# Optimization experiments

Hardware: AMD Instinct MI355X
Metric: run time of the kernel (lower is better)

The kernel has to match this reference:

```python
import jax, jax.numpy as jnp
import numpy as np

N_NODES = 20000
N_EDGES = 320000
T = 8
C_IN = 32
C_OUT = 32
C_EDGE = 16


def setup_inputs() -> dict:
    key = jax.random.key(0)
    ks = jax.random.split(key, 10)

    def xavier(k, shape):
        fan_in, fan_out = shape[0], shape[1]
        limit = float(np.sqrt(6.0 / (fan_in + fan_out)))
        return jax.random.uniform(k, shape, jnp.float32, -limit, limit)

    X = jax.random.normal(ks[0], (N_NODES, T, C_IN), jnp.float32)
    edge_index = jax.random.randint(ks[1], (2, N_EDGES), 0, N_NODES, jnp.int32)
    edge_attr = jax.random.normal(ks[2], (N_EDGES, C_EDGE), jnp.float32)
    Wn1 = xavier(ks[3], (C_IN, C_OUT))
    We1 = xavier(ks[4], (C_EDGE, C_OUT))
    u1 = xavier(ks[5], (C_OUT, C_OUT))
    Wn2 = xavier(ks[6], (C_OUT, C_OUT))
    We2 = xavier(ks[7], (C_EDGE, C_OUT))
    u2 = xavier(ks[8], (C_OUT, C_OUT))
    return {"X": X, "edge_index": edge_index, "edge_attr": edge_attr,
            "Wn1": Wn1, "We1": We1, "u1": u1,
            "Wn2": Wn2, "We2": We2, "u2": u2}


def _gat_conv(x, edge_index, edge_attr, Wn, We, u):
    # x: [N, T, C_in] -> h: [N, T, C_out]
    h = jnp.matmul(x, Wn)
    _ea = jnp.matmul(edge_attr, We)  # computed in original forward, unused in message (dead code)
    # per-edge matmul with u == node-level matmul then gather (same math, cheaper)
    hu = jnp.matmul(h, u)  # [N, T, C]
    src, tgt = edge_index[0], edge_index[1]
    x_j = hu[src]  # [E, T, C]
    x_i = hu[tgt]  # [E, T, C]
    gate = jax.nn.sigmoid(jnp.sum(x_i * x_j, axis=-1, keepdims=True))  # [E, T, 1]
    msg = x_j * gate  # [E, T, C]
    agg = jax.ops.segment_max(msg, tgt, num_segments=N_NODES)  # max-aggregate into targets
    agg = jnp.where(jnp.isfinite(agg), agg, jnp.zeros((), agg.dtype))  # empty segments -> 0 (PyG fill)
    return h + agg  # residual update


def reference(X, edge_index, edge_attr, Wn1, We1, u1, Wn2, We2, u2):
    c1 = jax.nn.leaky_relu(_gat_conv(X, edge_index, edge_attr, Wn1, We1, u1), 0.01)
    c2 = jax.nn.leaky_relu(_gat_conv(c1, edge_index, edge_attr, Wn2, We2, u2), 0.01)
    return c2
```

## Files before the change

### kernel.cpp

```cpp
#include <hip/hip_runtime.h>
#include <hip/hip_fp16.h>
#include <cstdint>
#include <cstddef>
#include <math.h>

#define NNODES 20000
#define NEDGES 320000
#define TDIM   8
#define CDIM   32
#define RROWS  (NNODES * TDIM)
#define NELEM  (RROWS * CDIM)
#define NODEB  79

static __device__ __forceinline__ unsigned pk2(float a, float b) {
    __half2 h = __floats2half2_rn(a, b);
    return *reinterpret_cast<unsigned*>(&h);
}

static __device__ __forceinline__ void cvt8(uint4 r, float* a) {
    float2 f;
    f = __half22float2(*reinterpret_cast<__half2*>(&r.x)); a[0] = f.x; a[1] = f.y;
    f = __half22float2(*reinterpret_cast<__half2*>(&r.y)); a[2] = f.x; a[3] = f.y;
    f = __half22float2(*reinterpret_cast<__half2*>(&r.z)); a[4] = f.x; a[5] = f.y;
    f = __half22float2(*reinterpret_cast<__half2*>(&r.w)); a[6] = f.x; a[7] = f.y;
}

__global__ __launch_bounds__(256) void init_kernel(
    const float* __restrict__ Wn1, const float* __restrict__ u1, float* __restrict__ WU1,
    const float* __restrict__ Wn2, const float* __restrict__ u2, float* __restrict__ WU2,
    int* __restrict__ counts)
{
    int blk = blockIdx.x, tid = threadIdx.x;
    if (blk < NODEB) {
        int i = blk * 256 + tid;
        if (i < NNODES) counts[i] = 0;
        return;
    }
    int b = blk - NODEB;
    const float* W  = (b < 4) ? Wn1 : Wn2;
    const float* U  = (b < 4) ? u1  : u2;
    float*       WU = (b < 4) ? WU1 : WU2;
    int idx = (b & 3) * 256 + tid;
    int k = idx >> 5, c = idx & 31;
    float acc = 0.f;
#pragma unroll
    for (int j = 0; j < CDIM; ++j) acc = fmaf(W[k * CDIM + j], U[j * CDIM + c], acc);
    WU[idx] = acc;
}

__global__ __launch_bounds__(256) void hist_kernel(
    const int* __restrict__ ei, int* __restrict__ counts)
{
    int e = blockIdx.x * 256 + threadIdx.x;
    if (e < NEDGES) atomicAdd(&counts[ei[NEDGES + e]], 1);
}

__global__ __launch_bounds__(256) void scan_kernel(
    const int* __restrict__ counts,
    int* __restrict__ offsets, int* __restrict__ cursor)
{
    __shared__ int sd[256];
    int blk = blockIdx.x, tid = threadIdx.x;

    int pre = 0;
    for (int i = tid; i < blk * 256; i += 256) pre += counts[i];
    sd[tid] = pre;
    __syncthreads();
#pragma unroll
    for (int off = 128; off > 0; off >>= 1) {
        if (tid < off) sd[tid] += sd[tid + off];
        __syncthreads();
    }
    int base = sd[0];
    __syncthreads();

    int i = blk * 256 + tid;
    int v = (i < NNODES) ? counts[i] : 0;
    sd[tid] = v;
    __syncthreads();
#pragma unroll
    for (int off = 1; off < 256; off <<= 1) {
        int t = (tid >= off) ? sd[tid - off] : 0;
        __syncthreads();
        sd[tid] += t;
        __syncthreads();
    }
    int excl = base + sd[tid] - v;
    if (i < NNODES) { offsets[i] = excl; cursor[i] = excl; }
    if (i == NNODES - 1) offsets[NNODES] = NEDGES;
}

__global__ __launch_bounds__(256) void scatter_kernel(
    const int* __restrict__ ei,
    int* __restrict__ cursor,
    int* __restrict__ csr_src)
{
    int e = blockIdx.x * 256 + threadIdx.x;
    if (e < NEDGES) {
        int t = ei[NEDGES + e];
        int pos = atomicAdd(&cursor[t], 1);
        csr_src[pos] = ei[e];
    }
}

template<bool IN16>
__global__ __launch_bounds__(256) void linear2_kernel(
    const void* __restrict__ inp,
    const float* __restrict__ W,
    const float* __restrict__ WU,
    __half* __restrict__ h16,
    __half* __restrict__ hu16)
{
    __shared__ float sx[64][33];
    int tid = threadIdx.x;
    int rowBase = blockIdx.x * 64;

    if (IN16) {
        const char* base = (const char*)inp + (size_t)rowBase * 64;
        uint4 v = *(const uint4*)(base + (size_t)tid * 16);
        float a[8];
        cvt8(v, a);
        int r = tid >> 2, q = tid & 3;
#pragma unroll
        for (int j = 0; j < 8; ++j) sx[r][q * 8 + j] = a[j];
    } else {
        const float4* in4 = (const float4*)((const float*)inp + (size_t)rowBase * CDIM);
#pragma unroll
        for (int i = 0; i < 2; ++i) {
            int idx = tid + i * 256;
            float4 v = in4[idx];
            int r = idx >> 3, q = idx & 7;
            sx[r][4 * q + 0] = v.x; sx[r][4 * q + 1] = v.y;
            sx[r][4 * q + 2] = v.z; sx[r][4 * q + 3] = v.w;
        }
    }
    __syncthreads();

    int lane  = tid & 63;
    int chunk = __builtin_amdgcn_readfirstlane(tid >> 6);
    int row = rowBase + lane;

    float hr[8], acc[8];
#pragma unroll
    for (int j = 0; j < 8; ++j) { hr[j] = 0.f; acc[j] = 0.f; }

    const float* Wc  = W  + chunk * 8;
    const float* WUc = WU + chunk * 8;
#pragma unroll 4
    for (int k = 0; k < CDIM; ++k) {
        float xk = sx[lane][k];
#pragma unroll
        for (int j = 0; j < 8; ++j) {
            hr[j]  = fmaf(xk, Wc[k * CDIM + j],  hr[j]);
            acc[j] = fmaf(xk, WUc[k * CDIM + j], acc[j]);
        }
    }

    uint4* hp = (uint4*)((char*)h16 + (size_t)row * 64 + chunk * 16);
    *hp = make_uint4(pk2(hr[0], hr[1]), pk2(hr[2], hr[3]),
                     pk2(hr[4], hr[5]), pk2(hr[6], hr[7]));

    uint4* up = (uint4*)((char*)hu16 + (size_t)row * 64 + chunk * 16);
    *up = make_uint4(pk2(acc[0], acc[1]), pk2(acc[2], acc[3]),
                     pk2(acc[4], acc[5]), pk2(acc[6], acc[7]));
}

template<bool OUT16>
__global__ __launch_bounds__(256) void agg_kernel(
    const int* __restrict__ offsets,
    const int* __restrict__ csr_src,
    const __half* __restrict__ hu16,
    const __half* __restrict__ h16,
    void* __restrict__ outp)
{
    int tid = threadIdx.x;
    int n = blockIdx.x * 4 + (tid >> 6);
    int l64 = tid & 63;
    int half = l64 >> 5;
    int l32 = l64 & 31;
    uint32_t rowOff = (uint32_t)l32 * 16u;
    const char* hub = (const char*)hu16;

    float b[8];
    cvt8(*(const uint4*)(hub + ((uint32_t)n << 9) + rowOff), b);

    int k0 = offsets[n];
    int k1 = offsets[n + 1];

    float m[8];
#pragma unroll
    for (int j = 0; j < 8; ++j) m[j] = -INFINITY;

    int k = k0;
    int e0 = 0, e1 = 0;
    if (k + 4 <= k1) {
        e0 = csr_src[k + half];
        e1 = csr_src[k + 2 + half];
    }
    while (k + 4 <= k1) {
        uint4 r0 = *(const uint4*)(hub + (((uint32_t)e0 << 9) + rowOff));
        uint4 r1 = *(const uint4*)(hub + (((uint32_t)e1 << 9) + rowOff));
        k += 4;
        if (k + 4 <= k1) {
            e0 = csr_src[k + half];
            e1 = csr_src[k + 2 + half];
        }
        float a0[8], a1[8];
        cvt8(r0, a0); cvt8(r1, a1);
        float q0 = 0.f, q1 = 0.f;
#pragma unroll
        for (int j = 0; j < 8; ++j) { q0 = fmaf(a0[j], b[j], q0); q1 = fmaf(a1[j], b[j], q1); }
        q0 += __shfl_xor(q0, 1); q1 += __shfl_xor(q1, 1);
        q0 += __shfl_xor(q0, 2); q1 += __shfl_xor(q1, 2);
        float g0 = 1.f / (1.f + __expf(-q0));
        float g1 = 1.f / (1.f + __expf(-q1));
#pragma unroll
        for (int j = 0; j < 8; ++j) {
            m[j] = fmaxf(m[j], a0[j] * g0);
            m[j] = fmaxf(m[j], a1[j] * g1);
        }
    }
    for (; k < k1; ++k) {
        int s = csr_src[k];
        float a0[8];
        cvt8(*(const uint4*)(hub + (((uint32_t)s << 9) + rowOff)), a0);
        float q0 = 0.f;
#pragma unroll
        for (int j = 0; j < 8; ++j) q0 = fmaf(a0[j], b[j], q0);
        q0 += __shfl_xor(q0, 1);
        q0 += __shfl_xor(q0, 2);
        float g0 = 1.f / (1.f + __expf(-q0));
#pragma unroll
        for (int j = 0; j < 8; ++j) m[j] = fmaxf(m[j], a0[j] * g0);
    }

#pragma unroll
    for (int j = 0; j < 8; ++j) m[j] = fmaxf(m[j], __shfl_xor(m[j], 32));

    if (half == 0) {
        bool has = (k1 > k0);
        float hv[8];
        cvt8(*(const uint4*)((const char*)h16 + ((uint32_t)n << 9) + rowOff), hv);
        float o[8];
#pragma unroll
        for (int j = 0; j < 8; ++j) {
            float a = has ? m[j] : 0.f;
            float vv = hv[j] + a;
            o[j] = (vv >= 0.f) ? vv : 0.01f * vv;
        }
        if (OUT16) {
            uint4 w = make_uint4(pk2(o[0], o[1]), pk2(o[2], o[3]),
                                 pk2(o[4], o[5]), pk2(o[6], o[7]));
            *(uint4*)((char*)outp + ((uint32_t)n << 9) + rowOff) = w;
        } else {
            uint32_t nodeOff = (uint32_t)n * 1024u + (uint32_t)l32 * 32u;
            char* ob = (char*)outp;
            *(float4*)(ob + nodeOff)      = make_float4(o[0], o[1], o[2], o[3]);
            *(float4*)(ob + nodeOff + 16) = make_float4(o[4], o[5], o[6], o[7]);
        }
    }
}

extern "C" void kernel_launch(void* const* d_in, const int* in_sizes, int n_in,
                              void* d_out, int out_size, void* d_ws, size_t ws_size,
                              hipStream_t stream)
{
    const float* X   = (const float*)d_in[0];
    const int*   ei  = (const int*)  d_in[1];
    const float* Wn1 = (const float*)d_in[3];
    const float* u1  = (const float*)d_in[5];
    const float* Wn2 = (const float*)d_in[6];
    const float* u2  = (const float*)d_in[8];

    int* counts  = (int*)d_ws;
    int* offsets = counts + NNODES;
    int* cursor  = offsets + NNODES + 1;
    float* WU1   = (float*)(cursor + NNODES);
    float* WU2   = WU1 + 1024;
    int* csr     = (int*)(WU2 + 1024);
    __half* A16  = (__half*)(((uintptr_t)(csr + NEDGES) + 255) & ~(uintptr_t)255);
    __half* Hh   = A16 + NELEM;
    __half* HU   = Hh + NELEM;

    const int linBlocks  = RROWS / 64;
    const int edgeBlocks = (NEDGES + 255) / 256;
    const int aggBlocks  = NNODES / 4;

    init_kernel<<<NODEB + 8, 256, 0, stream>>>(Wn1, u1, WU1, Wn2, u2, WU2, counts);
    hist_kernel<<<edgeBlocks, 256, 0, stream>>>(ei, counts);
    scan_kernel<<<NODEB, 256, 0, stream>>>(counts, offsets, cursor);
    scatter_kernel<<<edgeBlocks, 256, 0, stream>>>(ei, cursor, csr);

    linear2_kernel<false><<<linBlocks, 256, 0, stream>>>(X, Wn1, WU1, Hh, HU);
    agg_kernel<true><<<aggBlocks, 256, 0, stream>>>(offsets, csr, HU, Hh, A16);

    linear2_kernel<true><<<linBlocks, 256, 0, stream>>>(A16, Wn2, WU2, Hh, HU);
    agg_kernel<false><<<aggBlocks, 256, 0, stream>>>(offsets, csr, HU, Hh, d_out);
}
```

Measured before the change: 145.0 us.

## Fuse layer-1 aggregation with layer-2 linear transform in one kernel

Replaces the layer-1 aggregation kernel and the layer-2 linear kernel with a single fused kernel. Each 512-thread block aggregates 8 nodes, writes the leaky-relu output into shared memory, then computes the layer-2 h and hu projections directly from it. This drops the fp16 intermediate round trip through global memory and one kernel launch. Because the compute now follows a block-wide barrier, slow high-degree nodes can stall the whole block, and the larger 512-thread blocks may reduce occupancy.

```diff
diff --git a/kernel.cpp b/kernel.cpp
--- a/kernel.cpp
+++ b/kernel.cpp
@@ -103,9 +103,8 @@
     }
 }
 
-template<bool IN16>
 __global__ __launch_bounds__(256) void linear2_kernel(
-    const void* __restrict__ inp,
+    const float* __restrict__ in,
     const float* __restrict__ W,
     const float* __restrict__ WU,
     __half* __restrict__ h16,
@@ -115,24 +114,14 @@
     int tid = threadIdx.x;
     int rowBase = blockIdx.x * 64;
 
-    if (IN16) {
-        const char* base = (const char*)inp + (size_t)rowBase * 64;
-        uint4 v = *(const uint4*)(base + (size_t)tid * 16);
-        float a[8];
-        cvt8(v, a);
-        int r = tid >> 2, q = tid & 3;
-#pragma unroll
-        for (int j = 0; j < 8; ++j) sx[r][q * 8 + j] = a[j];
-    } else {
-        const float4* in4 = (const float4*)((const float*)inp + (size_t)rowBase * CDIM);
-#pragma unroll
-        for (int i = 0; i < 2; ++i) {
-            int idx = tid + i * 256;
-            float4 v = in4[idx];
-            int r = idx >> 3, q = idx & 7;
-            sx[r][4 * q + 0] = v.x; sx[r][4 * q + 1] = v.y;
-            sx[r][4 * q + 2] = v.z; sx[r][4 * q + 3] = v.w;
-        }
+    const float4* in4 = (const float4*)(in + (size_t)rowBase * CDIM);
+#pragma unroll
+    for (int i = 0; i < 2; ++i) {
+        int idx = tid + i * 256;
+        float4 v = in4[idx];
+        int r = idx >> 3, q = idx & 7;
+        sx[r][4 * q + 0] = v.x; sx[r][4 * q + 1] = v.y;
+        sx[r][4 * q + 2] = v.z; sx[r][4 * q + 3] = v.w;
     }
     __syncthreads();
 
@@ -159,19 +148,131 @@
     uint4* hp = (uint4*)((char*)h16 + (size_t)row * 64 + chunk * 16);
     *hp = make_uint4(pk2(hr[0], hr[1]), pk2(hr[2], hr[3]),
                      pk2(hr[4], hr[5]), pk2(hr[6], hr[7]));
-
     uint4* up = (uint4*)((char*)hu16 + (size_t)row * 64 + chunk * 16);
     *up = make_uint4(pk2(acc[0], acc[1]), pk2(acc[2], acc[3]),
                      pk2(acc[4], acc[5]), pk2(acc[6], acc[7]));
 }
 
-template<bool OUT16>
+__global__ __launch_bounds__(512) void aggfuse_kernel(
+    const int* __restrict__ offsets,
+    const int* __restrict__ csr_src,
+    const __half* __restrict__ hu16,
+    const __half* __restrict__ h16,
+    const float* __restrict__ W2,
+    const float* __restrict__ WU2,
+    __half* __restrict__ h2_16,
+    __half* __restrict__ hu2_16)
+{
+    __shared__ float sc1[64][33];
+    int tid = threadIdx.x;
+    int wid = tid >> 6;
+    int n = blockIdx.x * 8 + wid;
+    int l64 = tid & 63;
+    int half = l64 >> 5;
+    int l32 = l64 & 31;
+    uint32_t rowOff = (uint32_t)l32 * 16u;
+    const char* hub = (const char*)hu16;
+
+    float b[8];
+    cvt8(*(const uint4*)(hub + ((uint32_t)n << 9) + rowOff), b);
+
+    int k0 = offsets[n];
+    int k1 = offsets[n + 1];
+
+    float m[8];
+#pragma unroll
+    for (int j = 0; j < 8; ++j) m[j] = -INFINITY;
+
+    int k = k0;
+    int e0 = 0, e1 = 0;
+    if (k + 4 <= k1) {
+        e0 = csr_src[k + half];
+        e1 = csr_src[k + 2 + half];
+    }
+    while (k + 4 <= k1) {
+        uint4 r0 = *(const uint4*)(hub + (((uint32_t)e0 << 9) + rowOff));
+        uint4 r1 = *(const uint4*)(hub + (((uint32_t)e1 << 9) + rowOff));
+        k += 4;
+        if (k + 4 <= k1) {
+            e0 = csr_src[k + half];
+            e1 = csr_src[k + 2 + half];
+        }
+        float a0[8], a1[8];
+        cvt8(r0, a0); cvt8(r1, a1);
+        float q0 = 0.f, q1 = 0.f;
+#pragma unroll
+        for (int j = 0; j < 8; ++j) { q0 = fmaf(a0[j], b[j], q0); q1 = fmaf(a1[j], b[j], q1); }
+        q0 += __shfl_xor(q0, 1); q1 += __shfl_xor(q1, 1);
+        q0 += __shfl_xor(q0, 2); q1 += __shfl_xor(q1, 2);
+        float g0 = 1.f / (1.f + __expf(-q0));
+        float g1 = 1.f / (1.f + __expf(-q1));
+#pragma unroll
+        for (int j = 0; j < 8; ++j) {
+            m[j] = fmaxf(m[j], a0[j] * g0);
+            m[j] = fmaxf(m[j], a1[j] * g1);
+        }
+    }
+    for (; k < k1; ++k) {
+        int s = csr_src[k];
+        float a0[8];
+        cvt8(*(const uint4*)(hub + (((uint32_t)s << 9) + rowOff)), a0);
+        float q0 = 0.f;
+#pragma unroll
+        for (int j = 0; j < 8; ++j) q0 = fmaf(a0[j], b[j], q0);
+        q0 += __shfl_xor(q0, 1);
+        q0 += __shfl_xor(q0, 2);
+        float g0 = 1.f / (1.f + __expf(-q0));
+#pragma unroll
+        for (int j = 0; j < 8; ++j) m[j] = fmaxf(m[j], a0[j] * g0);
+    }
+
+#pragma unroll
+    for (int j = 0; j < 8; ++j) m[j] = fmaxf(m[j], __shfl_xor(m[j], 32));
+
+    if (half == 0) {
+        bool has = (k1 > k0);
+        float hv[8];
+        cvt8(*(const uint4*)((const char*)h16 + ((uint32_t)n << 9) + rowOff), hv);
+        int rloc = wid * 8 + (l32 >> 2);
+        int cbase = (l32 & 3) * 8;
+#pragma unroll
+        for (int j = 0; j < 8; ++j) {
+            float a = has ? m[j] : 0.f;
+            float vv = hv[j] + a;
+            sc1[rloc][cbase + j] = (vv >= 0.f) ? vv : 0.01f * vv;
+        }
+    }
+    __syncthreads();
+
+    int w = __builtin_amdgcn_readfirstlane(wid);
+    int r = l64;
+    float h2[4], a2[4];
+#pragma unroll
+    for (int j = 0; j < 4; ++j) { h2[j] = 0.f; a2[j] = 0.f; }
+
+    const float* Wc = W2  + w * 4;
+    const float* Uc = WU2 + w * 4;
+#pragma unroll 4
+    for (int kk = 0; kk < CDIM; ++kk) {
+        float xk = sc1[r][kk];
+#pragma unroll
+        for (int j = 0; j < 4; ++j) {
+            h2[j] = fmaf(xk, Wc[kk * CDIM + j], h2[j]);
+            a2[j] = fmaf(xk, Uc[kk * CDIM + j], a2[j]);
+        }
+    }
+
+    size_t rowg = (size_t)blockIdx.x * 64 + r;
+    *(uint2*)((char*)h2_16  + rowg * 64 + w * 8) = make_uint2(pk2(h2[0], h2[1]), pk2(h2[2], h2[3]));
+    *(uint2*)((char*)hu2_16 + rowg * 64 + w * 8) = make_uint2(pk2(a2[0], a2[1]), pk2(a2[2], a2[3]));
+}
+
 __global__ __launch_bounds__(256) void agg_kernel(
     const int* __restrict__ offsets,
     const int* __restrict__ csr_src,
     const __half* __restrict__ hu16,
     const __half* __restrict__ h16,
-    void* __restrict__ outp)
+    float* __restrict__ outp)
 {
     int tid = threadIdx.x;
     int n = blockIdx.x * 4 + (tid >> 6);
@@ -248,16 +349,10 @@
             float vv = hv[j] + a;
             o[j] = (vv >= 0.f) ? vv : 0.01f * vv;
         }
-        if (OUT16) {
-            uint4 w = make_uint4(pk2(o[0], o[1]), pk2(o[2], o[3]),
-                                 pk2(o[4], o[5]), pk2(o[6], o[7]));
-            *(uint4*)((char*)outp + ((uint32_t)n << 9) + rowOff) = w;
-        } else {
-            uint32_t nodeOff = (uint32_t)n * 1024u + (uint32_t)l32 * 32u;
-            char* ob = (char*)outp;
-            *(float4*)(ob + nodeOff)      = make_float4(o[0], o[1], o[2], o[3]);
-            *(float4*)(ob + nodeOff + 16) = make_float4(o[4], o[5], o[6], o[7]);
-        }
+        uint32_t nodeOff = (uint32_t)n * 1024u + (uint32_t)l32 * 32u;
+        char* ob = (char*)outp;
+        *(float4*)(ob + nodeOff)      = make_float4(o[0], o[1], o[2], o[3]);
+        *(float4*)(ob + nodeOff + 16) = make_float4(o[4], o[5], o[6], o[7]);
     }
 }
 
@@ -278,12 +373,14 @@
     float* WU1   = (float*)(cursor + NNODES);
     float* WU2   = WU1 + 1024;
     int* csr     = (int*)(WU2 + 1024);
-    __half* A16  = (__half*)(((uintptr_t)(csr + NEDGES) + 255) & ~(uintptr_t)255);
-    __half* Hh   = A16 + NELEM;
-    __half* HU   = Hh + NELEM;
+    __half* Hh1  = (__half*)(((uintptr_t)(csr + NEDGES) + 255) & ~(uintptr_t)255);
+    __half* HU1  = Hh1 + NELEM;
+    __half* Hh2  = HU1 + NELEM;
+    __half* HU2  = Hh2 + NELEM;
 
     const int linBlocks  = RROWS / 64;
     const int edgeBlocks = (NEDGES + 255) / 256;
+    const int fuseBlocks = NNODES / 8;
     const int aggBlocks  = NNODES / 4;
 
     init_kernel<<<NODEB + 8, 256, 0, stream>>>(Wn1, u1, WU1, Wn2, u2, WU2, counts);
@@ -291,9 +388,10 @@
     scan_kernel<<<NODEB, 256, 0, stream>>>(counts, offsets, cursor);
     scatter_kernel<<<edgeBlocks, 256, 0, stream>>>(ei, cursor, csr);
 
-    linear2_kernel<false><<<linBlocks, 256, 0, stream>>>(X, Wn1, WU1, Hh, HU);
-    agg_kernel<true><<<aggBlocks, 256, 0, stream>>>(offsets, csr, HU, Hh, A16);
-
-    linear2_kernel<true><<<linBlocks, 256, 0, stream>>>(A16, Wn2, WU2, Hh, HU);
-    agg_kernel<false><<<aggBlocks, 256, 0, stream>>>(offsets, csr, HU, Hh, d_out);
-}
+    linear2_kernel<<<linBlocks, 256, 0, stream>>>(X, Wn1, WU1, Hh1, HU1);
+
+    aggfuse_kernel<<<fuseBlocks, 512, 0, stream>>>(offsets, csr, HU1, Hh1,
+                                                   Wn2, WU2, Hh2, HU2);
+
+    agg_kernel<<<aggBlocks, 256, 0, stream>>>(offsets, csr, HU2, Hh2, (float*)d_out);
+}
```

New measurement: 138.5 us, median of 2. 4.5% less time.
